# Kernel optimization log

Measured on AMD Instinct MI355X. Metric: run time of the kernel, lower is better.

## Reference

```python
import jax, jax.numpy as jnp
import numpy as np

IN, OUT, B = 2048, 1000, 8192
EXP = (2048, 4096, 6144, 8192)
LN_EPS = 1e-5


def _mish(v):
    return v * jnp.tanh(jax.nn.softplus(v))


def _gelu(v):
    return jax.nn.gelu(v, approximate=False)  # torch F.gelu default is exact erf


def setup_inputs() -> dict:
    key = jax.random.key(0)
    ks = iter(jax.random.split(key, 48))
    nk = lambda: next(ks)
    r = lambda shape, s=0.02: jax.random.normal(nk(), shape, jnp.float32) * s
    d = {"x": jax.random.normal(nk(), (B, IN), jnp.float32)}
    d["W"] = r((OUT, IN), 0.05)
    d["b"] = r((OUT,), 0.01)
    for i, e in enumerate(EXP):
        d[f"up_w{i}"] = r((e, IN))
        d[f"down_w{i}"] = r((OUT, e))
        d[f"router_w{i}"] = r((i + 2, IN), 0.05)
        d[f"router_b{i}"] = r((i + 2,), 0.01)
    d["scales"] = r((4,), 0.1)
    d["ln_g"] = jnp.ones((IN,), jnp.float32)
    d["ln_b"] = jnp.zeros((IN,), jnp.float32)
    d["dom_router_w"] = r((4, IN), 0.05)
    d["dom_router_b"] = r((4,), 0.01)
    d["dom_experts_w"] = r((OUT * 4, IN))
    d["calib_w"] = r((OUT, IN))
    d["calib_b"] = r((OUT,), 0.01)
    d["rg_w1"] = r((IN // 4, IN))
    d["rg_w2"] = r((OUT, IN // 4))
    d["rg_b2"] = r((OUT,), 0.01)
    d["zeta"] = jnp.float32(0.5)
    d["theta"] = jnp.float32(0.5)
    d["lambda_"] = jnp.float32(0.5)
    return d


def _forward(x, W, b,
             up_w0, down_w0, router_w0, router_b0,
             up_w1, down_w1, router_w1, router_b1,
             up_w2, down_w2, router_w2, router_b2,
             up_w3, down_w3, router_w3, router_b3,
             scales, ln_g, ln_b,
             dom_router_w, dom_router_b, dom_experts_w,
             calib_w, calib_b, rg_w1, rg_w2, rg_b2,
             zeta, theta, lambda_):
    acts = (jax.nn.silu, _gelu, _mish, jax.nn.relu)
    ups = (up_w0, up_w1, up_w2, up_w3)
    downs = (down_w0, down_w1, down_w2, down_w3)
    r_ws = (router_w0, router_w1, router_w2, router_w3)
    r_bs = (router_b0, router_b1, router_b2, router_b3)

    base_logits = x @ W.T + b                      # [B, OUT]
    # dropout is identity (eval mode)
    branch_outs = [acts[i](x @ ups[i].T) @ downs[i].T for i in range(4)]  # each [B, OUT]

    final_mix = base_logits
    for i in range(4):
        route = jax.nn.softmax(x @ r_ws[i].T + r_bs[i], axis=-1)  # [B, i+2]
        # only first i+1 routing weights are used (faithful to source)
        mix = sum(route[..., j:j + 1] * branch_outs[j] for j in range(i + 1))
        final_mix = final_mix + scales[i] * mix

    # pre_norm (LayerNorm, eps=1e-5)
    mu = jnp.mean(x, axis=-1, keepdims=True)
    var = jnp.var(x, axis=-1, keepdims=True)
    h = (x - mu) * jax.lax.rsqrt(var + LN_EPS) * ln_g + ln_b

    dom_logits = (jax.nn.silu(h) @ dom_experts_w.T).reshape(h.shape[0], 4, OUT)
    dom_w = jax.nn.softmax(h @ dom_router_w.T + dom_router_b, axis=-1)[..., None]  # [B,4,1]
    dom_mix = jnp.sum(dom_w * dom_logits, axis=-2)                                 # [B,OUT]

    calib = jnp.tanh(h @ calib_w.T + calib_b)
    reason = jnp.tanh(jax.nn.silu(x @ rg_w1.T) @ rg_w2.T + rg_b2)
    return final_mix + zeta * dom_mix + theta * calib + lambda_ * reason


def reference(x, W, b,
              up_w0, down_w0, router_w0, router_b0,
              up_w1, down_w1, router_w1, router_b1,
              up_w2, down_w2, router_w2, router_b2,
              up_w3, down_w3, router_w3, router_b3,
              scales, ln_g, ln_b,
              dom_router_w, dom_router_b, dom_experts_w,
              calib_w, calib_b, rg_w1, rg_w2, rg_b2,
              zeta, theta, lambda_):
    return _forward(x, W, b,
                    up_w0, down_w0, router_w0, router_b0,
                    up_w1, down_w1, router_w1, router_b1,
                    up_w2, down_w2, router_w2, router_b2,
                    up_w3, down_w3, router_w3, router_b3,
                    scales, ln_g, ln_b,
                    dom_router_w, dom_router_b, dom_experts_w,
                    calib_w, calib_b, rg_w1, rg_w2, rg_b2,
                    zeta, theta, lambda_)
```

## Files before the change

### kernel.cpp

```cpp
#include <hip/hip_runtime.h>
#include <hip/hip_bf16.h>
#include <cstdint>
#include <cstddef>

#define DEVI __device__ __forceinline__

typedef short bf16x8 __attribute__((ext_vector_type(8)));
typedef float f32x4 __attribute__((ext_vector_type(4)));

static constexpr int B_ = 8192;
static constexpr int IN_ = 2048;
static constexpr int OUT_ = 1000;

DEVI float bf2f(unsigned short u) { return __uint_as_float(((unsigned int)u) << 16); }
DEVI unsigned short f2bf(float f) {
    unsigned int x = __float_as_uint(f);
    unsigned int r = x + 0x7FFFu + ((x >> 16) & 1u);
    return (unsigned short)(r >> 16);
}

DEVI void gload16(const unsigned short* g, unsigned short* l) {
    __builtin_amdgcn_global_load_lds((const __attribute__((address_space(1))) void*)g,
                                     (__attribute__((address_space(3))) void*)l, 16, 0, 0);
}

DEVI void xcd_swizzle(int& bx, int& by) {
    const int NX = gridDim.x, NY = gridDim.y;
    if ((NY & 7) == 0) {
        const int NYc = NY >> 3;
        const int d = by * NX + bx;
        const int xcd = d & 7, idx = d >> 3;
        by = xcd * NYc + (idx % NYc);
        bx = idx / NYc;
    }
}

DEVI float fast_tanh(float x) {
    float xc = fminf(fmaxf(x, -10.f), 10.f);
    float e = __expf(2.f * xc);
    return 1.f - 2.f / (e + 1.f);
}

template <int ACT> DEVI float apply_act(float v) {
    if constexpr (ACT == 1) return v / (1.f + __expf(-v));
    else if constexpr (ACT == 2) return 0.5f * v * (1.f + erff(v * 0.70710678118654752f));
    else if constexpr (ACT == 3) {
        float p = __expf(fminf(v, 20.f));
        float sp = (v > 20.f) ? v : __logf(1.f + p);
        return v * fast_tanh(sp);
    } else if constexpr (ACT == 4) return fmaxf(v, 0.f);
    else if constexpr (ACT == 5) return fast_tanh(v);
    else return v;
}

__global__ __launch_bounds__(256) void cvt_kernel(const float* __restrict__ in,
                                                  unsigned short* __restrict__ out, int n4) {
    int stride = gridDim.x * blockDim.x;
    for (int i = blockIdx.x * blockDim.x + threadIdx.x; i < n4; i += stride) {
        float4 v = ((const float4*)in)[i];
        ushort4 o;
        o.x = f2bf(v.x); o.y = f2bf(v.y); o.z = f2bf(v.z); o.w = f2bf(v.w);
        ((ushort4*)out)[i] = o;
    }
}

__global__ __launch_bounds__(256) void cvt_dom_kernel(const float* __restrict__ in,
                                                      unsigned short* __restrict__ out) {
    const int total = 4096 * (IN_ / 4);
    int stride = gridDim.x * blockDim.x;
    for (int i = blockIdx.x * blockDim.x + threadIdx.x; i < total; i += stride) {
        int orow = i >> 9;
        int oc4 = i & 511;
        int s = orow >> 10, r = orow & 1023;
        ushort4 o = {0, 0, 0, 0};
        if (r < 1000) {
            float4 v = ((const float4*)(in + ((size_t)(s * 1000 + r)) * IN_))[oc4];
            o.x = f2bf(v.x); o.y = f2bf(v.y); o.z = f2bf(v.z); o.w = f2bf(v.w);
        }
        ((ushort4*)out)[i] = o;
    }
}

__global__ __launch_bounds__(256) void stats_kernel(const float* __restrict__ x,
                                                    const float* __restrict__ g,
                                                    const float* __restrict__ bta,
                                                    float* __restrict__ mu,
                                                    float* __restrict__ rstd,
                                                    unsigned short* __restrict__ xb,
                                                    unsigned short* __restrict__ hb,
                                                    unsigned short* __restrict__ shb,
                                                    const int wX, const int wH, const int wS) {
    const int r = blockIdx.x;
    const int t = threadIdx.x;
    const float* xr = x + (size_t)r * IN_;
    float v[8];
    float s = 0.f, q = 0.f;
#pragma unroll
    for (int i = 0; i < 8; ++i) {
        v[i] = xr[t + i * 256];
        s += v[i];
        q += v[i] * v[i];
    }
#pragma unroll
    for (int off = 32; off > 0; off >>= 1) {
        s += __shfl_down(s, off);
        q += __shfl_down(q, off);
    }
    __shared__ float ss[4], qq[4];
    if ((t & 63) == 0) { ss[t >> 6] = s; qq[t >> 6] = q; }
    __syncthreads();
    s = ss[0] + ss[1] + ss[2] + ss[3];
    q = qq[0] + qq[1] + qq[2] + qq[3];
    const float mean = s * (1.f / IN_);
    const float var = q * (1.f / IN_) - mean * mean;
    const float rs = rsqrtf(var + 1e-5f);
    if (t == 0) { mu[r] = mean; rstd[r] = rs; }
#pragma unroll
    for (int i = 0; i < 8; ++i) {
        int c = t + i * 256;
        if (wX) xb[(size_t)r * IN_ + c] = f2bf(v[i]);
        if (wH | wS) {
            float h = (v[i] - mean) * rs * g[c] + bta[c];
            if (wH) hb[(size_t)r * IN_ + c] = f2bf(h);
            if (wS) shb[(size_t)r * IN_ + c] = f2bf(h / (1.f + __expf(-h)));
        }
    }
}

__global__ __launch_bounds__(256) void router_kernel(
    const float* __restrict__ x, const float* __restrict__ mu, const float* __restrict__ rstd,
    const float* __restrict__ g, const float* __restrict__ bta,
    const float* __restrict__ rw0, const float* __restrict__ rb0,
    const float* __restrict__ rw1, const float* __restrict__ rb1,
    const float* __restrict__ rw2, const float* __restrict__ rb2,
    const float* __restrict__ rw3, const float* __restrict__ rb3,
    const float* __restrict__ scales, const float* __restrict__ domw,
    const float* __restrict__ domb, float* __restrict__ coeff) {
    const int r = blockIdx.x;
    const int t = threadIdx.x;
    __shared__ float xs[IN_];
    __shared__ float hs[IN_];
    __shared__ float dots[18];
    const float m = mu[r], rs = rstd[r];
#pragma unroll
    for (int i = 0; i < 8; ++i) {
        int c = t + i * 256;
        float xv = x[(size_t)r * IN_ + c];
        xs[c] = xv;
        hs[c] = (xv - m) * rs * g[c] + bta[c];
    }
    __syncthreads();
    const int w = t >> 6, l = t & 63;
    const float* wp[5] = {rw0, rw1, rw2, rw3, domw};
    for (int d = w; d < 18; d += 4) {
        int gidx, row;
        if (d < 2) { gidx = 0; row = d; }
        else if (d < 5) { gidx = 1; row = d - 2; }
        else if (d < 9) { gidx = 2; row = d - 5; }
        else if (d < 14) { gidx = 3; row = d - 9; }
        else { gidx = 4; row = d - 14; }
        const float* wt = wp[gidx] + (size_t)row * IN_;
        const float* src = (gidx == 4) ? hs : xs;
        float p = 0.f;
        for (int i = l; i < IN_; i += 64) p += src[i] * wt[i];
#pragma unroll
        for (int off = 32; off > 0; off >>= 1) p += __shfl_down(p, off);
        if (l == 0) dots[d] = p;
    }
    __syncthreads();
    if (t == 0) {
        const float* rbs[4] = {rb0, rb1, rb2, rb3};
        float c[4] = {0.f, 0.f, 0.f, 0.f};
        int off = 0;
        for (int i = 0; i < 4; ++i) {
            int n = i + 2;
            float lg[5], mx = -1e30f;
            for (int j = 0; j < n; ++j) { lg[j] = dots[off + j] + rbs[i][j]; mx = fmaxf(mx, lg[j]); }
            float den = 0.f;
            for (int j = 0; j < n; ++j) { lg[j] = expf(lg[j] - mx); den += lg[j]; }
            float inv = 1.f / den;
            float sci = scales[i];
            for (int j = 0; j <= i; ++j) c[j] += sci * lg[j] * inv;
            off += n;
        }
        float dl[4], mx = -1e30f;
        for (int k = 0; k < 4; ++k) { dl[k] = dots[14 + k] + domb[k]; mx = fmaxf(mx, dl[k]); }
        float den = 0.f;
        for (int k = 0; k < 4; ++k) { dl[k] = expf(dl[k] - mx); den += dl[k]; }
        float inv = 1.f / den;
        for (int j = 0; j < 4; ++j) coeff[(size_t)r * 8 + j] = c[j];
        for (int k = 0; k < 4; ++k) coeff[(size_t)r * 8 + 4 + k] = dl[k] * inv;
    }
}

template <int ACT>
__global__ __launch_bounds__(512, 2) void gemm8p(
    const unsigned short* __restrict__ A, const unsigned short* __restrict__ Bw,
    unsigned short* __restrict__ outB, const int N, const int K) {
    extern __shared__ unsigned short lds[];
    const int t = threadIdx.x;
    const int l = t & 63, w = t >> 6;
    const int wr = w >> 2, wc = w & 3;
    int bx = blockIdx.x, by = blockIdx.y;
    xcd_swizzle(bx, by);
    const int rowBase = by * 256, colBase = bx * 256;

    const int lr = l >> 3;
    const int lcs = (((l & 7) ^ lr) << 3);
    const unsigned short* aSrc[4];
    const unsigned short* bSrc[4];
    int aDst[4], bDst[4];
#pragma unroll
    for (int j = 0; j < 4; ++j) {
        const int h = j >> 1, ci = w * 2 + (j & 1);
        aSrc[j] = A + (size_t)(rowBase + h * 128 + ci * 8 + lr) * K + lcs;
        bSrc[j] = Bw + (size_t)(colBase + h * 128 + ci * 8 + lr) * K + lcs;
        aDst[j] = h * 8192 + ci * 512;
        bDst[j] = 16384 + h * 8192 + ci * 512;
    }

    const int fr = l & 15, fg = l >> 4;
    const int kx0 = ((fg ^ (fr & 7)) << 3);
    const int kx1 = (((4 + fg) ^ (fr & 7)) << 3);
    const int aRow = (wr * 128 + fr) * 64;
    const int bRow = 16384 + (wc * 64 + fr) * 64;

    f32x4 acc[8][4];
#pragma unroll
    for (int m = 0; m < 8; ++m)
#pragma unroll
        for (int n = 0; n < 4; ++n) acc[m][n] = (f32x4){0.f, 0.f, 0.f, 0.f};

    const int nt = K >> 6;

#pragma unroll
    for (int j = 0; j < 4; ++j) gload16(aSrc[j], &lds[aDst[j]]);
#pragma unroll
    for (int j = 0; j < 4; ++j) gload16(bSrc[j], &lds[bDst[j]]);

    bf16x8 aF[4][2], bF[2][2];

#define LOAD_A(mh)                                                                         \
    _Pragma("unroll") for (int m = 0; m < 4; ++m) {                                        \
        aF[m][0] = *(const bf16x8*)&lds[bo + aRow + ((mh)*64 + m * 16) * 64 + kx0];        \
        aF[m][1] = *(const bf16x8*)&lds[bo + aRow + ((mh)*64 + m * 16) * 64 + kx1];        \
    }
#define LOAD_B(nh)                                                                         \
    _Pragma("unroll") for (int n = 0; n < 2; ++n) {                                        \
        bF[n][0] = *(const bf16x8*)&lds[bo + bRow + ((nh)*32 + n * 16) * 64 + kx0];        \
        bF[n][1] = *(const bf16x8*)&lds[bo + bRow + ((nh)*32 + n * 16) * 64 + kx1];        \
    }
#define MFMA_PHASE(mh, nh)                                                                 \
    __builtin_amdgcn_s_setprio(1);                                                         \
    _Pragma("unroll") for (int m = 0; m < 4; ++m)                                          \
        _Pragma("unroll") for (int n = 0; n < 2; ++n) {                                    \
            acc[(mh)*4 + m][(nh)*2 + n] = __builtin_amdgcn_mfma_f32_16x16x32_bf16(         \
                aF[m][0], bF[n][0], acc[(mh)*4 + m][(nh)*2 + n], 0, 0, 0);                 \
            acc[(mh)*4 + m][(nh)*2 + n] = __builtin_amdgcn_mfma_f32_16x16x32_bf16(         \
                aF[m][1], bF[n][1], acc[(mh)*4 + m][(nh)*2 + n], 0, 0, 0);                 \
        }                                                                                  \
    __builtin_amdgcn_s_setprio(0);

    for (int ti = 0; ti < nt; ++ti) {
        const int bo = (ti & 1) << 15;
        const int so = bo ^ 32768;
        const int ko = (ti + 1) << 6;
        const bool pre = (ti + 1 < nt);
        asm volatile("s_waitcnt vmcnt(0)" ::: "memory");
        asm volatile("s_barrier" ::: "memory");
        if (pre) {
#pragma unroll
            for (int j = 0; j < 4; ++j) gload16(aSrc[j] + ko, &lds[so + aDst[j]]);
        }
        LOAD_A(0)
        LOAD_B(0)
        MFMA_PHASE(0, 0)
        asm volatile("s_barrier" ::: "memory");
        if (pre) {
#pragma unroll
            for (int j = 0; j < 4; ++j) gload16(bSrc[j] + ko, &lds[so + bDst[j]]);
        }
        LOAD_A(1)
        MFMA_PHASE(1, 0)
        asm volatile("s_barrier" ::: "memory");
        LOAD_B(1)
        MFMA_PHASE(1, 1)
        asm volatile("s_barrier" ::: "memory");
        LOAD_A(0)
        MFMA_PHASE(0, 1)
    }
#undef LOAD_A
#undef LOAD_B
#undef MFMA_PHASE

#pragma unroll
    for (int m = 0; m < 8; ++m) {
        const int grow0 = rowBase + wr * 128 + m * 16 + fg * 4;
#pragma unroll
        for (int n = 0; n < 4; ++n) {
            const int gcol = colBase + wc * 64 + n * 16 + fr;
#pragma unroll
            for (int j = 0; j < 4; ++j) {
                float v = apply_act<ACT>(acc[m][n][j]);
                outB[(size_t)(grow0 + j) * N + gcol] = f2bf(v);
            }
        }
    }
}

template <int ACT, int MODE, int BIASF>
__global__ __launch_bounds__(256) void gemm_lds(
    const unsigned short* __restrict__ A, const unsigned short* __restrict__ Bw,
    float* __restrict__ outF, unsigned short* __restrict__ outB,
    const float* __restrict__ bias, const float* __restrict__ coeff, const int cidx,
    const float* __restrict__ scalarp, const int N, const int K) {
    __shared__ unsigned short Asm[2][4096];
    __shared__ unsigned short Bsm[2][4096];
    const int t = threadIdx.x;
    const int l = t & 63;
    const int w = t >> 6;
    const int wr = w >> 1, wc = w & 1;
    int bx = blockIdx.x, by = blockIdx.y;
    xcd_swizzle(bx, by);
    const int rowBase = by * 128;
    const int colBase = bx * 128;

    const int lr = l >> 2;
    const int lk = (l & 3) << 3;
    const int ar0 = rowBase + w * 32 + lr;
    const int ar1 = ar0 + 16;
    int br0 = colBase + w * 32 + lr;      if (br0 >= N) br0 = N - 1;
    int br1 = colBase + w * 32 + 16 + lr; if (br1 >= N) br1 = N - 1;
    const unsigned short* pA0 = A + (size_t)ar0 * K + lk;
    const unsigned short* pA1 = A + (size_t)ar1 * K + lk;
    const unsigned short* pB0 = Bw + (size_t)br0 * K + lk;
    const unsigned short* pB1 = Bw + (size_t)br1 * K + lk;
    const int ldsA0 = (w * 32) * 32;
    const int ldsA1 = (w * 32 + 16) * 32;

    f32x4 acc[4][4];
#pragma unroll
    for (int m = 0; m < 4; ++m)
#pragma unroll
        for (int n = 0; n < 4; ++n) acc[m][n] = (f32x4){0.f, 0.f, 0.f, 0.f};

    const int nK = K >> 5;

    auto stage = [&](int buf, int kt) {
        const int ko = kt << 5;
        gload16(pA0 + ko, &Asm[buf][ldsA0]);
        gload16(pA1 + ko, &Asm[buf][ldsA1]);
        gload16(pB0 + ko, &Bsm[buf][ldsA0]);
        gload16(pB1 + ko, &Bsm[buf][ldsA1]);
    };

    stage(0, 0);
    __syncthreads();

    const int fr = l & 15;
    const int fg = l >> 4;
    const int aoff = (wr * 64 + fr) * 32 + fg * 8;
    const int boff = (wc * 64 + fr) * 32 + fg * 8;

    int buf = 0;
    for (int kt = 0; kt < nK; ++kt) {
        if (kt + 1 < nK) stage(buf ^ 1, kt + 1);
        bf16x8 af[4], bfr[4];
#pragma unroll
        for (int m = 0; m < 4; ++m) af[m] = *(const bf16x8*)&Asm[buf][aoff + m * 512];
#pragma unroll
        for (int n = 0; n < 4; ++n) bfr[n] = *(const bf16x8*)&Bsm[buf][boff + n * 512];
#pragma unroll
        for (int m = 0; m < 4; ++m)
#pragma unroll
            for (int n = 0; n < 4; ++n)
                acc[m][n] = __builtin_amdgcn_mfma_f32_16x16x32_bf16(af[m], bfr[n], acc[m][n], 0, 0, 0);
        __syncthreads();
        buf ^= 1;
    }

    const float scal = scalarp ? scalarp[0] : 1.0f;
#pragma unroll
    for (int m = 0; m < 4; ++m) {
        const int grow0 = rowBase + wr * 64 + m * 16 + fg * 4;
#pragma unroll
        for (int n = 0; n < 4; ++n) {
            const int gcol = colBase + wc * 64 + n * 16 + fr;
            if constexpr (MODE == 3) {
                const int s = gcol >> 10, nn = gcol & 1023;
                if (nn < 1000) {
#pragma unroll
                    for (int j = 0; j < 4; ++j) {
                        const int grow = grow0 + j;
                        const float alpha = scal * coeff[(size_t)grow * 8 + 4 + s];
                        atomicAdd(&outF[(size_t)grow * OUT_ + nn], alpha * acc[m][n][j]);
                    }
                }
            } else if (gcol < N) {
                float bv = BIASF ? bias[gcol] : 0.f;
#pragma unroll
                for (int j = 0; j < 4; ++j) {
                    const int grow = grow0 + j;
                    float v = acc[m][n][j] + bv;
                    v = apply_act<ACT>(v);
                    float alpha = scal;
                    if (coeff) alpha *= coeff[(size_t)grow * 8 + cidx];
                    v *= alpha;
                    const size_t o = (size_t)grow * N + gcol;
                    if constexpr (MODE == 2) outB[o] = f2bf(v);
                    else if constexpr (MODE == 1) outF[o] += v;
                    else outF[o] = v;
                }
            }
        }
    }
}

template <int ASRC, int ASIL, int BSRC, int ACT, int OUTBF, int ACCUM, int BIASF>
__global__ __launch_bounds__(256) void gemm_bt(
    const void* __restrict__ Ap, const void* __restrict__ Bp,
    float* __restrict__ outF, unsigned short* __restrict__ outB,
    const float* __restrict__ bias, const float* __restrict__ coeff, const int cidx,
    const float* __restrict__ scalarp,
    const float* __restrict__ muP, const float* __restrict__ rsP,
    const float* __restrict__ lng, const float* __restrict__ lnb,
    const int N, const int K) {
    __shared__ unsigned short Asm[2][4096];
    __shared__ unsigned short Bsm[2][4096];
    const int t = threadIdx.x;
    const int l = t & 63;
    const int w = t >> 6;
    const int wr = w >> 1, wc = w & 1;
    int bx = blockIdx.x, by = blockIdx.y;
    xcd_swizzle(bx, by);
    const int rowBase = by * 128;
    const int colBase = bx * 128;

    const int srow = t >> 2;
    const int skol = (t & 3) << 3;
    const int arow0 = rowBase + srow;
    const int arow1 = arow0 + 64;
    int br0 = colBase + srow;        if (br0 >= N) br0 = N - 1;
    int br1 = colBase + srow + 64;   if (br1 >= N) br1 = N - 1;

    float mu0 = 0.f, rs0 = 1.f, mu1 = 0.f, rs1 = 1.f;
    if constexpr (ASRC == 2) {
        mu0 = muP[arow0]; rs0 = rsP[arow0];
        mu1 = muP[arow1]; rs1 = rsP[arow1];
    }

    auto ldA = [&](int row, float mu_, float rs_, int k0) -> bf16x8 {
        if constexpr (ASRC == 0) {
            bf16x8 v = *(const bf16x8*)((const unsigned short*)Ap + (size_t)row * K + k0);
            if constexpr (ASIL) {
                bf16x8 r;
#pragma unroll
                for (int i = 0; i < 8; ++i) {
                    float f = bf2f((unsigned short)v[i]);
                    r[i] = (short)f2bf(f / (1.f + __expf(-f)));
                }
                return r;
            }
            return v;
        } else {
            const float* f = (const float*)Ap + (size_t)row * K + k0;
            float4 v0 = *(const float4*)f;
            float4 v1 = *(const float4*)(f + 4);
            float vv[8] = {v0.x, v0.y, v0.z, v0.w, v1.x, v1.y, v1.z, v1.w};
            if constexpr (ASRC == 2) {
                float4 g0 = *(const float4*)(lng + k0), g1 = *(const float4*)(lng + k0 + 4);
                float4 b0 = *(const float4*)(lnb + k0), b1 = *(const float4*)(lnb + k0 + 4);
                float gg[8] = {g0.x, g0.y, g0.z, g0.w, g1.x, g1.y, g1.z, g1.w};
                float bb[8] = {b0.x, b0.y, b0.z, b0.w, b1.x, b1.y, b1.z, b1.w};
#pragma unroll
                for (int i = 0; i < 8; ++i) vv[i] = (vv[i] - mu_) * rs_ * gg[i] + bb[i];
            }
            if constexpr (ASIL) {
#pragma unroll
                for (int i = 0; i < 8; ++i) vv[i] = vv[i] / (1.f + __expf(-vv[i]));
            }
            bf16x8 r;
#pragma unroll
            for (int i = 0; i < 8; ++i) r[i] = (short)f2bf(vv[i]);
            return r;
        }
    };
    auto ldB = [&](int row, int k0) -> bf16x8 {
        if constexpr (BSRC == 0) {
            return *(const bf16x8*)((const unsigned short*)Bp + (size_t)row * K + k0);
        } else {
            const float* f = (const float*)Bp + (size_t)row * K + k0;
            float4 v0 = *(const float4*)f;
            float4 v1 = *(const float4*)(f + 4);
            float vv[8] = {v0.x, v0.y, v0.z, v0.w, v1.x, v1.y, v1.z, v1.w};
            bf16x8 r;
#pragma unroll
            for (int i = 0; i < 8; ++i) r[i] = (short)f2bf(vv[i]);
            return r;
        }
    };

    const int wo = t * 8;

    f32x4 acc[4][4];
#pragma unroll
    for (int m = 0; m < 4; ++m)
#pragma unroll
        for (int n = 0; n < 4; ++n) acc[m][n] = (f32x4){0.f, 0.f, 0.f, 0.f};

    const int nK = K >> 5;

    bf16x8 a0 = ldA(arow0, mu0, rs0, skol);
    bf16x8 a1 = ldA(arow1, mu1, rs1, skol);
    bf16x8 b0 = ldB(br0, skol);
    bf16x8 b1 = ldB(br1, skol);
    *(bf16x8*)&Asm[0][wo] = a0; *(bf16x8*)&Asm[0][wo + 2048] = a1;
    *(bf16x8*)&Bsm[0][wo] = b0; *(bf16x8*)&Bsm[0][wo + 2048] = b1;
    __syncthreads();

    const int fr = l & 15;
    const int fg = l >> 4;
    const int aoff = (wr * 64 + fr) * 32 + fg * 8;
    const int boff = (wc * 64 + fr) * 32 + fg * 8;

    for (int kt = 0; kt < nK; ++kt) {
        const int cur = kt & 1;
        if (kt + 1 < nK) {
            const int ko = ((kt + 1) << 5) + skol;
            a0 = ldA(arow0, mu0, rs0, ko);
            a1 = ldA(arow1, mu1, rs1, ko);
            b0 = ldB(br0, ko);
            b1 = ldB(br1, ko);
        }
        bf16x8 af[4], bfr[4];
#pragma unroll
        for (int m = 0; m < 4; ++m) af[m] = *(const bf16x8*)&Asm[cur][aoff + m * 512];
#pragma unroll
        for (int n = 0; n < 4; ++n) bfr[n] = *(const bf16x8*)&Bsm[cur][boff + n * 512];
#pragma unroll
        for (int m = 0; m < 4; ++m)
#pragma unroll
            for (int n = 0; n < 4; ++n)
                acc[m][n] = __builtin_amdgcn_mfma_f32_16x16x32_bf16(af[m], bfr[n], acc[m][n], 0, 0, 0);
        if (kt + 1 < nK) {
            __syncthreads();
            const int nxt = cur ^ 1;
            *(bf16x8*)&Asm[nxt][wo] = a0; *(bf16x8*)&Asm[nxt][wo + 2048] = a1;
            *(bf16x8*)&Bsm[nxt][wo] = b0; *(bf16x8*)&Bsm[nxt][wo + 2048] = b1;
            __syncthreads();
        }
    }

    const float scal = scalarp ? scalarp[0] : 1.0f;
#pragma unroll
    for (int m = 0; m < 4; ++m) {
        const int grow0 = rowBase + wr * 64 + m * 16 + fg * 4;
#pragma unroll
        for (int n = 0; n < 4; ++n) {
            const int gcol = colBase + wc * 64 + n * 16 + fr;
            if (gcol < N) {
                float bv = BIASF ? bias[gcol] : 0.f;
#pragma unroll
                for (int j = 0; j < 4; ++j) {
                    const int grow = grow0 + j;
                    float v = acc[m][n][j] + bv;
                    v = apply_act<ACT>(v);
                    float alpha = scal;
                    if (coeff) alpha *= coeff[(size_t)grow * 8 + cidx];
                    v *= alpha;
                    const size_t o = (size_t)grow * N + gcol;
                    if (OUTBF) outB[o] = f2bf(v);
                    else if (ACCUM) outF[o] += v;
                    else outF[o] = v;
                }
            }
        }
    }
}

static inline void cvt(const float* in, unsigned short* out, size_t n, hipStream_t s) {
    int n4 = (int)(n >> 2);
    int blocks = (n4 + 255) / 256;
    if (blocks > 4096) blocks = 4096;
    cvt_kernel<<<blocks, 256, 0, s>>>(in, out, n4);
}

extern "C" void kernel_launch(void* const* d_in, const int* in_sizes, int n_in,
                              void* d_out, int out_size, void* d_ws, size_t ws_size,
                              hipStream_t stream) {
    (void)in_sizes; (void)n_in; (void)out_size;
    const float* x = (const float*)d_in[0];
    const float* W = (const float*)d_in[1];
    const float* bvec = (const float*)d_in[2];
    const float* up_w[4] = {(const float*)d_in[3], (const float*)d_in[7], (const float*)d_in[11], (const float*)d_in[15]};
    const float* down_w[4] = {(const float*)d_in[4], (const float*)d_in[8], (const float*)d_in[12], (const float*)d_in[16]};
    const float* r_w[4] = {(const float*)d_in[5], (const float*)d_in[9], (const float*)d_in[13], (const float*)d_in[17]};
    const float* r_b[4] = {(const float*)d_in[6], (const float*)d_in[10], (const float*)d_in[14], (const float*)d_in[18]};
    const float* scales = (const float*)d_in[19];
    const float* ln_g = (const float*)d_in[20];
    const float* ln_b = (const float*)d_in[21];
    const float* dom_rw = (const float*)d_in[22];
    const float* dom_rb = (const float*)d_in[23];
    const float* dom_ew = (const float*)d_in[24];
    const float* cal_w = (const float*)d_in[25];
    const float* cal_b = (const float*)d_in[26];
    const float* rg_w1 = (const float*)d_in[27];
    const float* rg_w2 = (const float*)d_in[28];
    const float* rg_b2 = (const float*)d_in[29];
    const float* zeta = (const float*)d_in[30];
    const float* theta = (const float*)d_in[31];
    const float* lam = (const float*)d_in[32];
    float* out = (float*)d_out;

    const int E[4] = {2048, 4096, 6144, 8192};
    auto al = [](size_t v) { return (v + 255) & ~(size_t)255; };

    size_t fastNeed = al((size_t)B_ * 8 * 4) + 2 * al((size_t)B_ * 4) +
                      2 * al((size_t)B_ * IN_ * 2) +
                      al((size_t)OUT_ * IN_ * 2) +
                      al((size_t)4096 * IN_ * 2) +
                      al((size_t)OUT_ * IN_ * 2) +
                      al((size_t)512 * IN_ * 2) + al((size_t)OUT_ * 512 * 2) +
                      al((size_t)B_ * 8192 * 2) + al((size_t)B_ * 512 * 2);
    for (int j = 0; j < 4; ++j)
        fastNeed += al((size_t)E[j] * IN_ * 2) + al((size_t)OUT_ * E[j] * 2);

    char* p = (char*)d_ws;
    auto alloc = [&](size_t bytes) { char* r = p; p += (bytes + 255) & ~(size_t)255; return r; };

    const int NT_OUT = (OUT_ + 127) / 128;
    const int MT = B_ / 128;

    if (ws_size >= fastNeed) {
        float* coeff = (float*)alloc((size_t)B_ * 8 * 4);
        float* muP = (float*)alloc((size_t)B_ * 4);
        float* rsP = (float*)alloc((size_t)B_ * 4);
        unsigned short* xb = (unsigned short*)alloc((size_t)B_ * IN_ * 2);
        unsigned short* shb = (unsigned short*)alloc((size_t)B_ * IN_ * 2);
        unsigned short* Wb = (unsigned short*)alloc((size_t)OUT_ * IN_ * 2);
        unsigned short* domN = (unsigned short*)alloc((size_t)4096 * IN_ * 2);
        unsigned short* calb = (unsigned short*)alloc((size_t)OUT_ * IN_ * 2);
        unsigned short* rg1b = (unsigned short*)alloc((size_t)512 * IN_ * 2);
        unsigned short* rg2b = (unsigned short*)alloc((size_t)OUT_ * 512 * 2);
        unsigned short* U = (unsigned short*)alloc((size_t)B_ * 8192 * 2);
        unsigned short* T = (unsigned short*)alloc((size_t)B_ * 512 * 2);
        unsigned short* upb[4];
        unsigned short* downb[4];
        for (int j = 0; j < 4; ++j) {
            upb[j] = (unsigned short*)alloc((size_t)E[j] * IN_ * 2);
            downb[j] = (unsigned short*)alloc((size_t)OUT_ * E[j] * 2);
        }
        unsigned short* hbU = U;

        hipFuncSetAttribute((const void*)gemm8p<1>, hipFuncAttributeMaxDynamicSharedMemorySize, 131072);
        hipFuncSetAttribute((const void*)gemm8p<2>, hipFuncAttributeMaxDynamicSharedMemorySize, 131072);
        hipFuncSetAttribute((const void*)gemm8p<3>, hipFuncAttributeMaxDynamicSharedMemorySize, 131072);
        hipFuncSetAttribute((const void*)gemm8p<4>, hipFuncAttributeMaxDynamicSharedMemorySize, 131072);

        cvt(W, Wb, (size_t)OUT_ * IN_, stream);
        cvt_dom_kernel<<<4096, 256, 0, stream>>>(dom_ew, domN);
        cvt(cal_w, calb, (size_t)OUT_ * IN_, stream);
        cvt(rg_w1, rg1b, (size_t)512 * IN_, stream);
        cvt(rg_w2, rg2b, (size_t)OUT_ * 512, stream);
        for (int j = 0; j < 4; ++j) {
            cvt(up_w[j], upb[j], (size_t)E[j] * IN_, stream);
            cvt(down_w[j], downb[j], (size_t)OUT_ * E[j], stream);
        }

        stats_kernel<<<B_, 256, 0, stream>>>(x, ln_g, ln_b, muP, rsP, xb, hbU, shb, 1, 1, 1);
        router_kernel<<<B_, 256, 0, stream>>>(x, muP, rsP, ln_g, ln_b,
                                              r_w[0], r_b[0], r_w[1], r_b[1], r_w[2], r_b[2],
                                              r_w[3], r_b[3], scales, dom_rw, dom_rb, coeff);

        gemm_lds<0, 0, 1><<<dim3(NT_OUT, MT), 256, 0, stream>>>(
            xb, Wb, out, nullptr, bvec, nullptr, 0, nullptr, OUT_, IN_);

        gemm_lds<0, 3, 0><<<dim3(32, MT), 256, 0, stream>>>(
            shb, domN, out, nullptr, nullptr, coeff, 0, zeta, 4096, IN_);

        gemm_lds<5, 1, 1><<<dim3(NT_OUT, MT), 256, 0, stream>>>(
            hbU, calb, out, nullptr, cal_b, nullptr, 0, theta, OUT_, IN_);

        gemm8p<1><<<dim3(E[0] / 256, B_ / 256), 512, 131072, stream>>>(xb, upb[0], U, E[0], IN_);
        gemm_lds<0, 1, 0><<<dim3(NT_OUT, MT), 256, 0, stream>>>(
            U, downb[0], out, nullptr, nullptr, coeff, 0, nullptr, OUT_, E[0]);
        gemm8p<2><<<dim3(E[1] / 256, B_ / 256), 512, 131072, stream>>>(xb, upb[1], U, E[1], IN_);
        gemm_lds<0, 1, 0><<<dim3(NT_OUT, MT), 256, 0, stream>>>(
            U, downb[1], out, nullptr, nullptr, coeff, 1, nullptr, OUT_, E[1]);
        gemm8p<3><<<dim3(E[2] / 256, B_ / 256), 512, 131072, stream>>>(xb, upb[2], U, E[2], IN_);
        gemm_lds<0, 1, 0><<<dim3(NT_OUT, MT), 256, 0, stream>>>(
            U, downb[2], out, nullptr, nullptr, coeff, 2, nullptr, OUT_, E[2]);
        gemm8p<4><<<dim3(E[3] / 256, B_ / 256), 512, 131072, stream>>>(xb, upb[3], U, E[3], IN_);
        gemm_lds<0, 1, 0><<<dim3(NT_OUT, MT), 256, 0, stream>>>(
            U, downb[3], out, nullptr, nullptr, coeff, 3, nullptr, OUT_, E[3]);

        gemm_lds<1, 2, 0><<<dim3(4, MT), 256, 0, stream>>>(
            xb, rg1b, nullptr, T, nullptr, nullptr, 0, nullptr, 512, IN_);
        gemm_lds<5, 1, 1><<<dim3(NT_OUT, MT), 256, 0, stream>>>(
            T, rg2b, out, nullptr, rg_b2, nullptr, 0, lam, OUT_, 512);
        return;
    }

    const size_t S_coeff = al((size_t)B_ * 8 * 4);
    const size_t S_mu = al((size_t)B_ * 4);
    const size_t S_act = al((size_t)B_ * IN_ * 2);
    size_t S_W = al((size_t)OUT_ * IN_ * 2) + al((size_t)4 * OUT_ * IN_ * 2) +
                 al((size_t)OUT_ * IN_ * 2) + al((size_t)512 * IN_ * 2) + al((size_t)OUT_ * 512 * 2);
    for (int j = 0; j < 4; ++j) S_W += al((size_t)E[j] * IN_ * 2) + al((size_t)OUT_ * E[j] * 2);

    auto needOf = [&](bool bfl, bool cwl, int ch) {
        size_t n = S_coeff + 2 * S_mu;
        if (bfl) n += 3 * S_act;
        if (cwl) n += S_W;
        n += al((size_t)ch * 8192 * 2) + al((size_t)ch * 512 * 2);
        return n;
    };
    bool bf = false, cw = false;
    int CH = 512;
    {
        const bool cb[7] = {true, true, true, true, true, true, false};
        const bool cc[7] = {true, true, true, false, false, false, false};
        const int  cch[7] = {8192, 4096, 2048, 4096, 2048, 512, 512};
        for (int i = 0; i < 7; ++i) {
            if (needOf(cb[i], cc[i], cch[i]) <= ws_size || i == 6) {
                bf = cb[i]; cw = cc[i]; CH = cch[i];
                break;
            }
        }
    }

    float* coeff = (float*)alloc((size_t)B_ * 8 * 4);
    float* muP = (float*)alloc((size_t)B_ * 4);
    float* rsP = (float*)alloc((size_t)B_ * 4);
    unsigned short *xb = nullptr, *hb = nullptr, *shb = nullptr;
    if (bf) {
        xb = (unsigned short*)alloc((size_t)B_ * IN_ * 2);
        hb = (unsigned short*)alloc((size_t)B_ * IN_ * 2);
        shb = (unsigned short*)alloc((size_t)B_ * IN_ * 2);
    }
    unsigned short *Wb = nullptr, *upb[4] = {}, *downb[4] = {}, *domb_ = nullptr,
                   *calb = nullptr, *rg1b = nullptr, *rg2b = nullptr;
    if (cw) {
        Wb = (unsigned short*)alloc((size_t)OUT_ * IN_ * 2);
        domb_ = (unsigned short*)alloc((size_t)4 * OUT_ * IN_ * 2);
        calb = (unsigned short*)alloc((size_t)OUT_ * IN_ * 2);
        rg1b = (unsigned short*)alloc((size_t)512 * IN_ * 2);
        rg2b = (unsigned short*)alloc((size_t)OUT_ * 512 * 2);
        for (int j = 0; j < 4; ++j) {
            upb[j] = (unsigned short*)alloc((size_t)E[j] * IN_ * 2);
            downb[j] = (unsigned short*)alloc((size_t)OUT_ * E[j] * 2);
        }
    }
    unsigned short* U = (unsigned short*)alloc((size_t)CH * 8192 * 2);
    unsigned short* T = (unsigned short*)alloc((size_t)CH * 512 * 2);

    if (cw) {
        cvt(W, Wb, (size_t)OUT_ * IN_, stream);
        for (int j = 0; j < 4; ++j) {
            cvt(up_w[j], upb[j], (size_t)E[j] * IN_, stream);
            cvt(down_w[j], downb[j], (size_t)OUT_ * E[j], stream);
        }
        cvt(dom_ew, domb_, (size_t)4 * OUT_ * IN_, stream);
        cvt(cal_w, calb, (size_t)OUT_ * IN_, stream);
        cvt(rg_w1, rg1b, (size_t)512 * IN_, stream);
        cvt(rg_w2, rg2b, (size_t)OUT_ * 512, stream);
    }

    stats_kernel<<<B_, 256, 0, stream>>>(x, ln_g, ln_b, muP, rsP, xb, hb, shb,
                                         bf ? 1 : 0, bf ? 1 : 0, bf ? 1 : 0);
    router_kernel<<<B_, 256, 0, stream>>>(x, muP, rsP, ln_g, ln_b,
                                          r_w[0], r_b[0], r_w[1], r_b[1], r_w[2], r_b[2],
                                          r_w[3], r_b[3], scales, dom_rw, dom_rb, coeff);

#define GARG(A, BW, OF, OB, BI, CF, CI, SC, MU, NN, KK) \
    (const void*)(A), (const void*)(BW), OF, OB, BI, CF, CI, SC, MU, rsP, ln_g, ln_b, NN, KK
#define LX(ACT, OUTBF, ACCUM, BIASF, GRID, Abf, Af, Bb, Bf, OF, OB, BI, CF, CI, SC, MU, NN, KK)         \
    do {                                                                                                \
        if (bf) {                                                                                       \
            if (cw) gemm_bt<0, 0, 0, ACT, OUTBF, ACCUM, BIASF><<<GRID, 256, 0, stream>>>(               \
                GARG(Abf, Bb, OF, OB, BI, CF, CI, SC, MU, NN, KK));                                     \
            else gemm_bt<0, 0, 1, ACT, OUTBF, ACCUM, BIASF><<<GRID, 256, 0, stream>>>(                  \
                GARG(Abf, Bf, OF, OB, BI, CF, CI, SC, MU, NN, KK));                                     \
        } else gemm_bt<1, 0, 1, ACT, OUTBF, ACCUM, BIASF><<<GRID, 256, 0, stream>>>(                    \
                GARG(Af, Bf, OF, OB, BI, CF, CI, SC, MU, NN, KK));                                      \
    } while (0)
#define LD(ACT, OUTBF, ACCUM, BIASF, GRID, A, Bb, Bf, OF, OB, BI, CF, CI, SC, NN, KK)                   \
    do {                                                                                                \
        if (cw) gemm_bt<0, 0, 0, ACT, OUTBF, ACCUM, BIASF><<<GRID, 256, 0, stream>>>(                   \
            GARG(A, Bb, OF, OB, BI, CF, CI, SC, muP, NN, KK));                                          \
        else gemm_bt<0, 0, 1, ACT, OUTBF, ACCUM, BIASF><<<GRID, 256, 0, stream>>>(                      \
            GARG(A, Bf, OF, OB, BI, CF, CI, SC, muP, NN, KK));                                          \
    } while (0)

    LX(0, 0, 0, 1, dim3(NT_OUT, MT), xb, x, Wb, W, out, nullptr, bvec, (const float*)nullptr, 0,
       (const float*)nullptr, muP, OUT_, IN_);

    for (int k = 0; k < 4; ++k) {
        const unsigned short* Bb = cw ? domb_ + (size_t)k * OUT_ * IN_ : nullptr;
        const float* Bf = dom_ew + (size_t)k * OUT_ * IN_;
        if (bf) {
            if (cw) gemm_bt<0, 0, 0, 0, 0, 1, 0><<<dim3(NT_OUT, MT), 256, 0, stream>>>(
                GARG(shb, Bb, out, nullptr, nullptr, coeff, 4 + k, zeta, muP, OUT_, IN_));
            else gemm_bt<0, 0, 1, 0, 0, 1, 0><<<dim3(NT_OUT, MT), 256, 0, stream>>>(
                GARG(shb, Bf, out, nullptr, nullptr, coeff, 4 + k, zeta, muP, OUT_, IN_));
        } else {
            gemm_bt<2, 1, 1, 0, 0, 1, 0><<<dim3(NT_OUT, MT), 256, 0, stream>>>(
                GARG(x, Bf, out, nullptr, nullptr, coeff, 4 + k, zeta, muP, OUT_, IN_));
        }
    }

    if (bf) {
        if (cw) gemm_bt<0, 0, 0, 5, 0, 1, 1><<<dim3(NT_OUT, MT), 256, 0, stream>>>(
            GARG(hb, calb, out, nullptr, cal_b, nullptr, 0, theta, muP, OUT_, IN_));
        else gemm_bt<0, 0, 1, 5, 0, 1, 1><<<dim3(NT_OUT, MT), 256, 0, stream>>>(
            GARG(hb, cal_w, out, nullptr, cal_b, nullptr, 0, theta, muP, OUT_, IN_));
    } else {
        gemm_bt<2, 0, 1, 5, 0, 1, 1><<<dim3(NT_OUT, MT), 256, 0, stream>>>(
            GARG(x, cal_w, out, nullptr, cal_b, nullptr, 0, theta, muP, OUT_, IN_));
    }

    for (int r0 = 0; r0 < B_; r0 += CH) {
        const int MTC = CH / 128;
        const unsigned short* xbC = bf ? xb + (size_t)r0 * IN_ : nullptr;
        const float* xC = x + (size_t)r0 * IN_;
        float* outC = out + (size_t)r0 * OUT_;
        const float* coeffC = coeff + (size_t)r0 * 8;
        for (int j = 0; j < 4; ++j) {
            dim3 gu(E[j] / 128, MTC);
            if (j == 0)
                LX(1, 1, 0, 0, gu, xbC, xC, upb[0], up_w[0], nullptr, U, nullptr, (const float*)nullptr, 0,
                   (const float*)nullptr, muP, E[0], IN_);
            else if (j == 1)
                LX(2, 1, 0, 0, gu, xbC, xC, upb[1], up_w[1], nullptr, U, nullptr, (const float*)nullptr, 0,
                   (const float*)nullptr, muP, E[1], IN_);
            else if (j == 2)
                LX(3, 1, 0, 0, gu, xbC, xC, upb[2], up_w[2], nullptr, U, nullptr, (const float*)nullptr, 0,
                   (const float*)nullptr, muP, E[2], IN_);
            else
                LX(4, 1, 0, 0, gu, xbC, xC, upb[3], up_w[3], nullptr, U, nullptr, (const float*)nullptr, 0,
                   (const float*)nullptr, muP, E[3], IN_);
            LD(0, 0, 1, 0, dim3(NT_OUT, MTC), U, downb[j], down_w[j], outC, nullptr, nullptr,
               coeffC, j, (const float*)nullptr, OUT_, E[j]);
        }
        LX(1, 1, 0, 0, dim3(4, MTC), xbC, xC, rg1b, rg_w1, nullptr, T, nullptr, (const float*)nullptr, 0,
           (const float*)nullptr, muP, 512, IN_);
        LD(5, 0, 1, 1, dim3(NT_OUT, MTC), T, rg2b, rg_w2, outC, nullptr, rg_b2, nullptr, 0, lam, OUT_, 512);
    }
#undef LX
#undef LD
#undef GARG
}
```

Measured before the change: 2.140 ms.

## Fuse base, calib and reasoning heads into one GEMM; drop dom atomics

```diff
diff --git a/kernel.cpp b/kernel.cpp
--- a/kernel.cpp
+++ b/kernel.cpp
@@ -386,17 +386,7 @@
 #pragma unroll
         for (int n = 0; n < 4; ++n) {
             const int gcol = colBase + wc * 64 + n * 16 + fr;
-            if constexpr (MODE == 3) {
-                const int s = gcol >> 10, nn = gcol & 1023;
-                if (nn < 1000) {
-#pragma unroll
-                    for (int j = 0; j < 4; ++j) {
-                        const int grow = grow0 + j;
-                        const float alpha = scal * coeff[(size_t)grow * 8 + 4 + s];
-                        atomicAdd(&outF[(size_t)grow * OUT_ + nn], alpha * acc[m][n][j]);
-                    }
-                }
-            } else if (gcol < N) {
+            if (gcol < N) {
                 float bv = BIASF ? bias[gcol] : 0.f;
 #pragma unroll
                 for (int j = 0; j < 4; ++j) {
@@ -411,6 +401,249 @@
                     else if constexpr (MODE == 1) outF[o] += v;
                     else outF[o] = v;
                 }
+            }
+        }
+    }
+}
+
+__global__ __launch_bounds__(256) void dom_kernel(
+    const unsigned short* __restrict__ A, const unsigned short* __restrict__ Bw,
+    float* __restrict__ outF, const float* __restrict__ coeff,
+    const float* __restrict__ zetap) {
+    constexpr int K = IN_;
+    constexpr int nK = K >> 5;
+    constexpr int nG = 4 * nK;
+    __shared__ unsigned short Asm[2][4096];
+    __shared__ unsigned short Bsm[2][4096];
+    const int t = threadIdx.x;
+    const int l = t & 63;
+    const int w = t >> 6;
+    const int wr = w >> 1, wc = w & 1;
+    int bx = blockIdx.x, by = blockIdx.y;
+    xcd_swizzle(bx, by);
+    const int rowBase = by * 128;
+    const int colBase = bx * 128;
+
+    const int lr = l >> 2;
+    const int lk = (l & 3) << 3;
+    const unsigned short* pA0 = A + (size_t)(rowBase + w * 32 + lr) * K + lk;
+    const unsigned short* pA1 = A + (size_t)(rowBase + w * 32 + 16 + lr) * K + lk;
+    const unsigned short* pB0 = Bw + (size_t)(colBase + w * 32 + lr) * K + lk;
+    const unsigned short* pB1 = Bw + (size_t)(colBase + w * 32 + 16 + lr) * K + lk;
+    const int ldsA0 = (w * 32) * 32;
+    const int ldsA1 = (w * 32 + 16) * 32;
+
+    f32x4 acc[4][4], res[4][4];
+#pragma unroll
+    for (int m = 0; m < 4; ++m)
+#pragma unroll
+        for (int n = 0; n < 4; ++n) {
+            acc[m][n] = (f32x4){0.f, 0.f, 0.f, 0.f};
+            res[m][n] = (f32x4){0.f, 0.f, 0.f, 0.f};
+        }
+
+    auto stage = [&](int buf, int g) {
+        const int kt = g & (nK - 1);
+        const int s = g >> 6;
+        const size_t ko = (size_t)kt << 5;
+        const size_t bo = ((size_t)s << 10) * K + ko;
+        gload16(pA0 + ko, &Asm[buf][ldsA0]);
+        gload16(pA1 + ko, &Asm[buf][ldsA1]);
+        gload16(pB0 + bo, &Bsm[buf][ldsA0]);
+        gload16(pB1 + bo, &Bsm[buf][ldsA1]);
+    };
+
+    stage(0, 0);
+    __syncthreads();
+
+    const int fr = l & 15;
+    const int fg = l >> 4;
+    const int aoff = (wr * 64 + fr) * 32 + fg * 8;
+    const int boff = (wc * 64 + fr) * 32 + fg * 8;
+
+    int buf = 0;
+    for (int g = 0; g < nG; ++g) {
+        if (g + 1 < nG) stage(buf ^ 1, g + 1);
+        bf16x8 af[4], bfr[4];
+#pragma unroll
+        for (int m = 0; m < 4; ++m) af[m] = *(const bf16x8*)&Asm[buf][aoff + m * 512];
+#pragma unroll
+        for (int n = 0; n < 4; ++n) bfr[n] = *(const bf16x8*)&Bsm[buf][boff + n * 512];
+#pragma unroll
+        for (int m = 0; m < 4; ++m)
+#pragma unroll
+            for (int n = 0; n < 4; ++n)
+                acc[m][n] = __builtin_amdgcn_mfma_f32_16x16x32_bf16(af[m], bfr[n], acc[m][n], 0, 0, 0);
+        if ((g & (nK - 1)) == nK - 1) {
+            const int s = g >> 6;
+#pragma unroll
+            for (int m = 0; m < 4; ++m) {
+                const int grow0 = rowBase + wr * 64 + m * 16 + fg * 4;
+#pragma unroll
+                for (int j = 0; j < 4; ++j) {
+                    const float ws = coeff[(size_t)(grow0 + j) * 8 + 4 + s];
+#pragma unroll
+                    for (int n = 0; n < 4; ++n) {
+                        res[m][n][j] += ws * acc[m][n][j];
+                        acc[m][n][j] = 0.f;
+                    }
+                }
+            }
+        }
+        __syncthreads();
+        buf ^= 1;
+    }
+
+    const float zeta = zetap[0];
+#pragma unroll
+    for (int m = 0; m < 4; ++m) {
+        const int grow0 = rowBase + wr * 64 + m * 16 + fg * 4;
+#pragma unroll
+        for (int n = 0; n < 4; ++n) {
+            const int gcol = colBase + wc * 64 + n * 16 + fr;
+            if (gcol < OUT_) {
+#pragma unroll
+                for (int j = 0; j < 4; ++j)
+                    outF[(size_t)(grow0 + j) * OUT_ + gcol] += zeta * res[m][n][j];
+            }
+        }
+    }
+}
+
+__global__ __launch_bounds__(256) void fused_head(
+    const unsigned short* __restrict__ Axb, const unsigned short* __restrict__ Ah,
+    const unsigned short* __restrict__ At,
+    const unsigned short* __restrict__ Bw, const unsigned short* __restrict__ Bc,
+    const unsigned short* __restrict__ Br,
+    float* __restrict__ outF, const float* __restrict__ bvec,
+    const float* __restrict__ calB, const float* __restrict__ rgB,
+    const float* __restrict__ thetap, const float* __restrict__ lamp) {
+    constexpr int nG = 64 + 64 + 16;
+    __shared__ unsigned short Asm[2][4096];
+    __shared__ unsigned short Bsm[2][4096];
+    const int t = threadIdx.x;
+    const int l = t & 63;
+    const int w = t >> 6;
+    const int wr = w >> 1, wc = w & 1;
+    int bx = blockIdx.x, by = blockIdx.y;
+    xcd_swizzle(bx, by);
+    const int rowBase = by * 128;
+    const int colBase = bx * 128;
+
+    const int lr = l >> 2;
+    const int lk = (l & 3) << 3;
+    const int ar0 = rowBase + w * 32 + lr;
+    const int ar1 = ar0 + 16;
+    int br0 = colBase + w * 32 + lr;      if (br0 >= OUT_) br0 = OUT_ - 1;
+    int br1 = colBase + w * 32 + 16 + lr; if (br1 >= OUT_) br1 = OUT_ - 1;
+    const unsigned short* a0r0 = Axb + (size_t)ar0 * 2048 + lk;
+    const unsigned short* a0r1 = Axb + (size_t)ar1 * 2048 + lk;
+    const unsigned short* a1r0 = Ah + (size_t)ar0 * 2048 + lk;
+    const unsigned short* a1r1 = Ah + (size_t)ar1 * 2048 + lk;
+    const unsigned short* a2r0 = At + (size_t)ar0 * 512 + lk;
+    const unsigned short* a2r1 = At + (size_t)ar1 * 512 + lk;
+    const unsigned short* b0r0 = Bw + (size_t)br0 * 2048 + lk;
+    const unsigned short* b0r1 = Bw + (size_t)br1 * 2048 + lk;
+    const unsigned short* b1r0 = Bc + (size_t)br0 * 2048 + lk;
+    const unsigned short* b1r1 = Bc + (size_t)br1 * 2048 + lk;
+    const unsigned short* b2r0 = Br + (size_t)br0 * 512 + lk;
+    const unsigned short* b2r1 = Br + (size_t)br1 * 512 + lk;
+    const int ldsA0 = (w * 32) * 32;
+    const int ldsA1 = (w * 32 + 16) * 32;
+
+    f32x4 acc[4][4], res[4][4];
+#pragma unroll
+    for (int m = 0; m < 4; ++m)
+#pragma unroll
+        for (int n = 0; n < 4; ++n) {
+            acc[m][n] = (f32x4){0.f, 0.f, 0.f, 0.f};
+            res[m][n] = (f32x4){0.f, 0.f, 0.f, 0.f};
+        }
+
+    auto stage = [&](int buf, int g) {
+        const int seg = (g < 64) ? 0 : ((g < 128) ? 1 : 2);
+        const int kt = g - ((seg == 0) ? 0 : ((seg == 1) ? 64 : 128));
+        const size_t ko = (size_t)kt << 5;
+        const unsigned short* A0 = (seg == 0) ? a0r0 : ((seg == 1) ? a1r0 : a2r0);
+        const unsigned short* A1 = (seg == 0) ? a0r1 : ((seg == 1) ? a1r1 : a2r1);
+        const unsigned short* B0 = (seg == 0) ? b0r0 : ((seg == 1) ? b1r0 : b2r0);
+        const unsigned short* B1 = (seg == 0) ? b0r1 : ((seg == 1) ? b1r1 : b2r1);
+        gload16(A0 + ko, &Asm[buf][ldsA0]);
+        gload16(A1 + ko, &Asm[buf][ldsA1]);
+        gload16(B0 + ko, &Bsm[buf][ldsA0]);
+        gload16(B1 + ko, &Bsm[buf][ldsA1]);
+    };
+
+    stage(0, 0);
+    __syncthreads();
+
+    const int fr = l & 15;
+    const int fg = l >> 4;
+    const int aoff = (wr * 64 + fr) * 32 + fg * 8;
+    const int boff = (wc * 64 + fr) * 32 + fg * 8;
+    const float theta = thetap[0], lam = lamp[0];
+
+    int buf = 0;
+    for (int g = 0; g < nG; ++g) {
+        if (g + 1 < nG) stage(buf ^ 1, g + 1);
+        bf16x8 af[4], bfr[4];
+#pragma unroll
+        for (int m = 0; m < 4; ++m) af[m] = *(const bf16x8*)&Asm[buf][aoff + m * 512];
+#pragma unroll
+        for (int n = 0; n < 4; ++n) bfr[n] = *(const bf16x8*)&Bsm[buf][boff + n * 512];
+#pragma unroll
+        for (int m = 0; m < 4; ++m)
+#pragma unroll
+            for (int n = 0; n < 4; ++n)
+                acc[m][n] = __builtin_amdgcn_mfma_f32_16x16x32_bf16(af[m], bfr[n], acc[m][n], 0, 0, 0);
+        if (g == 63) {
+#pragma unroll
+            for (int m = 0; m < 4; ++m)
+#pragma unroll
+                for (int n = 0; n < 4; ++n) {
+                    res[m][n] = acc[m][n];
+                    acc[m][n] = (f32x4){0.f, 0.f, 0.f, 0.f};
+                }
+        } else if (g == 127) {
+#pragma unroll
+            for (int n = 0; n < 4; ++n) {
+                int gc = colBase + wc * 64 + n * 16 + fr;
+                if (gc >= OUT_) gc = OUT_ - 1;
+                const float cb = calB[gc];
+#pragma unroll
+                for (int m = 0; m < 4; ++m)
+#pragma unroll
+                    for (int j = 0; j < 4; ++j) {
+                        res[m][n][j] += theta * fast_tanh(acc[m][n][j] + cb);
+                        acc[m][n][j] = 0.f;
+                    }
+            }
+        }
+        __syncthreads();
+        buf ^= 1;
+    }
+#pragma unroll
+    for (int n = 0; n < 4; ++n) {
+        int gc = colBase + wc * 64 + n * 16 + fr;
+        if (gc >= OUT_) gc = OUT_ - 1;
+        const float rb = rgB[gc];
+#pragma unroll
+        for (int m = 0; m < 4; ++m)
+#pragma unroll
+            for (int j = 0; j < 4; ++j) res[m][n][j] += lam * fast_tanh(acc[m][n][j] + rb);
+    }
+
+#pragma unroll
+    for (int m = 0; m < 4; ++m) {
+        const int grow0 = rowBase + wr * 64 + m * 16 + fg * 4;
+#pragma unroll
+        for (int n = 0; n < 4; ++n) {
+            const int gcol = colBase + wc * 64 + n * 16 + fr;
+            if (gcol < OUT_) {
+                const float bv = bvec[gcol];
+#pragma unroll
+                for (int j = 0; j < 4; ++j)
+                    outF[(size_t)(grow0 + j) * OUT_ + gcol] = res[m][n][j] + bv;
             }
         }
     }
@@ -672,14 +905,13 @@
                                               r_w[0], r_b[0], r_w[1], r_b[1], r_w[2], r_b[2],
                                               r_w[3], r_b[3], scales, dom_rw, dom_rb, coeff);
 
-        gemm_lds<0, 0, 1><<<dim3(NT_OUT, MT), 256, 0, stream>>>(
-            xb, Wb, out, nullptr, bvec, nullptr, 0, nullptr, OUT_, IN_);
-
-        gemm_lds<0, 3, 0><<<dim3(32, MT), 256, 0, stream>>>(
-            shb, domN, out, nullptr, nullptr, coeff, 0, zeta, 4096, IN_);
-
-        gemm_lds<5, 1, 1><<<dim3(NT_OUT, MT), 256, 0, stream>>>(
-            hbU, calb, out, nullptr, cal_b, nullptr, 0, theta, OUT_, IN_);
+        gemm_lds<1, 2, 0><<<dim3(4, MT), 256, 0, stream>>>(
+            xb, rg1b, nullptr, T, nullptr, nullptr, 0, nullptr, 512, IN_);
+
+        fused_head<<<dim3(NT_OUT, MT), 256, 0, stream>>>(
+            xb, hbU, T, Wb, calb, rg2b, out, bvec, cal_b, rg_b2, theta, lam);
+
+        dom_kernel<<<dim3(NT_OUT, MT), 256, 0, stream>>>(shb, domN, out, coeff, zeta);
 
         gemm8p<1><<<dim3(E[0] / 256, B_ / 256), 512, 131072, stream>>>(xb, upb[0], U, E[0], IN_);
         gemm_lds<0, 1, 0><<<dim3(NT_OUT, MT), 256, 0, stream>>>(
@@ -693,11 +925,6 @@
         gemm8p<4><<<dim3(E[3] / 256, B_ / 256), 512, 131072, stream>>>(xb, upb[3], U, E[3], IN_);
         gemm_lds<0, 1, 0><<<dim3(NT_OUT, MT), 256, 0, stream>>>(
             U, downb[3], out, nullptr, nullptr, coeff, 3, nullptr, OUT_, E[3]);
-
-        gemm_lds<1, 2, 0><<<dim3(4, MT), 256, 0, stream>>>(
-            xb, rg1b, nullptr, T, nullptr, nullptr, 0, nullptr, 512, IN_);
-        gemm_lds<5, 1, 1><<<dim3(NT_OUT, MT), 256, 0, stream>>>(
-            T, rg2b, out, nullptr, rg_b2, nullptr, 0, lam, OUT_, 512);
         return;
     }
 
```

Result: slower. 2.649 ms (+23.8%).
